# Optimization experiments

Hardware: AMD Instinct MI355X
Metric: run time of the kernel (lower is better)

Reference implementation:

```python
import jax, jax.numpy as jnp
import numpy as np

NUM_USERS, NUM_ITEMS, RANK = 610, 193609, 4
BATCH = 2097152


def setup_inputs() -> dict:
    key = jax.random.key(0)
    ks = jax.random.split(key, 10)
    users = jax.random.randint(ks[0], (BATCH,), 0, NUM_USERS + 1)
    items = jax.random.randint(ks[1], (BATCH,), 0, NUM_ITEMS + 1)
    # embedding tables (nn.Embedding default init ~ N(0,1))
    embed_U = jax.random.normal(ks[2], (NUM_USERS + 1, RANK), dtype=jnp.float32)
    embed_V = jax.random.normal(ks[3], (NUM_ITEMS + 1, RANK), dtype=jnp.float32)
    # Linear params, Kaiming-uniform-ish scale (1/sqrt(fan_in))
    def lin(k, fan_in, fan_out):
        k1, k2 = jax.random.split(k)
        bound = 1.0 / np.sqrt(fan_in)
        W = jax.random.uniform(k1, (fan_out, fan_in), jnp.float32, -bound, bound)
        b = jax.random.uniform(k2, (fan_out,), jnp.float32, -bound, bound)
        return W, b
    W1, b1 = lin(ks[4], 2 * RANK, 50)
    W2, b2 = lin(ks[5], 50, 20)
    W3, b3 = lin(ks[6], 20, 1)
    return {"users": users, "items": items,
            "embed_U": embed_U, "embed_V": embed_V,
            "W1": W1, "b1": b1, "W2": W2, "b2": b2, "W3": W3, "b3": b3}


def reference(users, items, embed_U, embed_V, W1, b1, W2, b2, W3, b3):
    # Vectorized version of the per-sample loop: gather + concat + 3-layer MLP
    eu = embed_U[users]                      # [B, rank]
    ev = embed_V[items]                      # [B, rank]
    x = jnp.concatenate([eu, ev], axis=-1)   # [B, 2*rank]
    x = jax.nn.relu(x @ W1.T + b1)           # [B, 50]
    x = jax.nn.relu(x @ W2.T + b2)           # [B, 20]
    x = x @ W3.T + b3                        # [B, 1]
    return x[:, 0]                           # [B]
```

## Files before the change

### kernel.cpp

```cpp
#include <hip/hip_runtime.h>
#include <hip/hip_fp16.h>


typedef __attribute__((ext_vector_type(16))) float    f32x16;
typedef __attribute__((ext_vector_type(8)))  _Float16 f16x8;
typedef __attribute__((ext_vector_type(2)))  _Float16 f16x2;
typedef __attribute__((ext_vector_type(2)))  __fp16   h16x2;

#define H1 50
#define H2 20

union W4 { unsigned u[4]; f16x8 v; };
union W8 { _Float16 h[8]; f16x8 v; };

static __device__ inline unsigned pk_u32(float a, float b) {
    h16x2 p = __builtin_amdgcn_cvt_pkrtz(a, b);
    unsigned u; __builtin_memcpy(&u, &p, 4); return u;
}
static __device__ inline unsigned pkmax0(unsigned a) {
    unsigned r;
    asm("v_pk_max_f16 %0, %1, %2" : "=v"(r) : "v"(a), "v"(0u));
    return r;
}
static __device__ inline float dot2(unsigned a, unsigned b, float c) {
    f16x2 av, bv;
    __builtin_memcpy(&av, &a, 4);
    __builtin_memcpy(&bv, &b, 4);
    return __builtin_amdgcn_fdot2(av, bv, c, false);
}

__global__ __launch_bounds__(256, 4) void neumf_mfma32(
    const int* __restrict__ users, const int* __restrict__ items,
    const float* __restrict__ eU, const float* __restrict__ eV,
    const float* __restrict__ W1, const float* __restrict__ b1,
    const float* __restrict__ W2, const float* __restrict__ b2,
    const float* __restrict__ W3, const float* __restrict__ b3,
    float* __restrict__ out, int n, int nTiles, int tilesPerWave, int nU)
{
    const int lane = threadIdx.x & 63;
    const int wid  = blockIdx.x * (blockDim.x >> 6) + (threadIdx.x >> 6);
    const int h    = lane >> 5;
    const int r31  = lane & 31;

    __shared__ uint2 ldsU[616];
    for (int r = threadIdx.x; r < nU; r += 256) {
        float4 t = reinterpret_cast<const float4*>(eU)[r];
        ldsU[r] = make_uint2(pk_u32(t.x, t.y), pk_u32(t.z, t.w));
    }
    __syncthreads();

    f16x8 a1[2];
#pragma unroll
    for (int mt = 0; mt < 2; ++mt) {
        int m = 32 * mt + r31;
        float w[8] = {0.f,0.f,0.f,0.f,0.f,0.f,0.f,0.f};
        if (m < H1) {
#pragma unroll
            for (int i = 0; i < 4; ++i) w[i] = W1[m * 8 + 4 * h + i];
            if (h == 0) w[4] = b1[m];
        }
        W8 f;
#pragma unroll
        for (int i = 0; i < 8; ++i) f.h[i] = (_Float16)w[i];
        a1[mt] = f.v;
    }

    f16x8 a2[4];
    {
        int m = r31;
#pragma unroll
        for (int kt = 0; kt < 4; ++kt) {
            float w[8] = {0.f,0.f,0.f,0.f,0.f,0.f,0.f,0.f};
            if (m < H2) {
#pragma unroll
                for (int e = 0; e < 8; ++e) {
                    int k = 16 * kt + 4 * h + (e & 3) + 8 * (e >> 2);
                    if (k < H1)       w[e] = W2[m * H1 + k];
                    else if (k == H1) w[e] = b2[m];
                }
            }
            W8 f;
#pragma unroll
            for (int e = 0; e < 8; ++e) f.h[e] = (_Float16)w[e];
            a2[kt] = f.v;
        }
    }

    f16x8 a3;
    {
        W8 f;
#pragma unroll
        for (int e = 0; e < 8; ++e) {
            int k = 4 * h + (e & 3) + 8 * (e >> 2);
            f.h[e] = (_Float16)W3[k];
        }
        a3 = f.v;
    }
    const unsigned w3p0 = h ? 0u : pk_u32(W3[16], W3[17]);
    const unsigned w3p1 = h ? 0u : pk_u32(W3[18], W3[19]);
    const float bias3 = b3[0];

    const int*     ip  = h ? items : users;
    const unsigned w2c = h ? 0u : 0x00003C00u;

    const int t0 = wid * tilesPerWave;
    const int t1 = min(t0 + tilesPerWave, nTiles);
    if (t0 >= t1) return;
    const int tl = t1 - 1;

    int idx_cur = ip[32 * t0 + r31];
    float4 gv_cur;
    if (h) gv_cur = *reinterpret_cast<const float4*>(eV + 4 * (size_t)idx_cur);
    int idx_next = ip[32 * min(t0 + 1, tl) + r31];

#pragma unroll 2
    for (int T = t0; T < t1; ++T) {
        float4 gv_next;
        if (h) gv_next = *reinterpret_cast<const float4*>(eV + 4 * (size_t)idx_next);
        int idx_nn = ip[32 * min(T + 2, tl) + r31];

        uint2 cw;
        if (h) cw = make_uint2(pk_u32(gv_cur.x, gv_cur.y), pk_u32(gv_cur.z, gv_cur.w));
        else   cw = ldsU[idx_cur];

        W4 bf1;
        bf1.u[0] = cw.x;
        bf1.u[1] = cw.y;
        bf1.u[2] = w2c;
        bf1.u[3] = 0u;

        f32x16 z = {0.f,0.f,0.f,0.f,0.f,0.f,0.f,0.f,0.f,0.f,0.f,0.f,0.f,0.f,0.f,0.f};
        f32x16 d1[2];
        d1[0] = __builtin_amdgcn_mfma_f32_32x32x16_f16(a1[0], bf1.v, z, 0, 0, 0);
        d1[1] = __builtin_amdgcn_mfma_f32_32x32x16_f16(a1[1], bf1.v, z, 0, 0, 0);

        f32x16 d2 = z;
#pragma unroll
        for (int kt = 0; kt < 3; ++kt) {
            const int mt = kt >> 1, q = kt & 1;
            W4 bf;
#pragma unroll
            for (int j = 0; j < 4; ++j)
                bf.u[j] = pkmax0(pk_u32(d1[mt][8 * q + 2 * j], d1[mt][8 * q + 2 * j + 1]));
            d2 = __builtin_amdgcn_mfma_f32_32x32x16_f16(a2[kt], bf.v, d2, 0, 0, 0);
        }
        {
            W4 bf;
            bf.u[0] = pkmax0(pk_u32(d1[1][8], d1[1][9]));
            bf.u[1] = w2c;
            bf.u[2] = w2c;
            bf.u[3] = w2c;
            d2 = __builtin_amdgcn_mfma_f32_32x32x16_f16(a2[3], bf.v, d2, 0, 0, 0);
        }

        W4 b3f;
        b3f.u[0] = pkmax0(pk_u32(d2[0], d2[1]));
        b3f.u[1] = pkmax0(pk_u32(d2[2], d2[3]));
        b3f.u[2] = pkmax0(pk_u32(d2[4], d2[5]));
        b3f.u[3] = pkmax0(pk_u32(d2[6], d2[7]));
        f32x16 d3 = __builtin_amdgcn_mfma_f32_32x32x16_f16(a3, b3f.v, z, 0, 0, 0);

        unsigned t0w = pkmax0(pk_u32(d2[8],  d2[9]));
        unsigned t1w = pkmax0(pk_u32(d2[10], d2[11]));
        float pt = dot2(t0w, w3p0, dot2(t1w, w3p1, bias3));

        if (!h) out[32 * T + r31] = d3[0] + pt;

        gv_cur = gv_next; idx_cur = idx_next; idx_next = idx_nn;
    }
}

extern "C" void kernel_launch(void* const* d_in, const int* in_sizes, int n_in,
                              void* d_out, int out_size, void* d_ws, size_t ws_size,
                              hipStream_t stream) {
    const int*   users = (const int*)d_in[0];
    const int*   items = (const int*)d_in[1];
    const float* eU    = (const float*)d_in[2];
    const float* eV    = (const float*)d_in[3];
    const float* W1    = (const float*)d_in[4];
    const float* b1    = (const float*)d_in[5];
    const float* W2    = (const float*)d_in[6];
    const float* b2    = (const float*)d_in[7];
    const float* W3    = (const float*)d_in[8];
    const float* b3    = (const float*)d_in[9];
    float*       out   = (float*)d_out;

    int n  = in_sizes[0];
    int nU = in_sizes[2] / 4;

    int nTiles = (n + 31) / 32;
    int blocks = 1024, threads = 256;
    int totalWaves = blocks * (threads / 64);
    int tilesPerWave = (nTiles + totalWaves - 1) / totalWaves;
    neumf_mfma32<<<blocks, threads, 0, stream>>>(users, items, eU, eV,
                                                 W1, b1, W2, b2, W3, b3,
                                                 out, n, nTiles, tilesPerWave, nU);
}
```

Before: 23.60 us.

## Process two 32-sample tiles per iteration to interleave independent MFMA chains

Each wave iteration now handles two independent 32-row tiles (A and B) and interleaves their MFMA chains, so one tile's MFMAs can issue while the other's dependent results are pending. Outputs are merged with a cross-half shuffle so all 64 lanes write a contiguous 64-element store instead of half the lanes writing 32. Launch bounds drop to 3 waves/SIMD and the grid goes from 1024 to 768 blocks to fit the higher register use. The cost is more VGPR pressure and lower occupancy, which may reduce latency hiding for the embedding gathers.

```diff
diff --git a/kernel.cpp b/kernel.cpp
--- a/kernel.cpp
+++ b/kernel.cpp
@@ -29,13 +29,13 @@
     return __builtin_amdgcn_fdot2(av, bv, c, false);
 }
 
-__global__ __launch_bounds__(256, 4) void neumf_mfma32(
+__global__ __launch_bounds__(256, 3) void neumf_dual(
     const int* __restrict__ users, const int* __restrict__ items,
     const float* __restrict__ eU, const float* __restrict__ eV,
     const float* __restrict__ W1, const float* __restrict__ b1,
     const float* __restrict__ W2, const float* __restrict__ b2,
     const float* __restrict__ W3, const float* __restrict__ b3,
-    float* __restrict__ out, int n, int nTiles, int tilesPerWave, int nU)
+    float* __restrict__ out, int n, int nIter, int itersPerWave, int nU)
 {
     const int lane = threadIdx.x & 63;
     const int wid  = blockIdx.x * (blockDim.x >> 6) + (threadIdx.x >> 6);
@@ -103,70 +103,102 @@
     const int*     ip  = h ? items : users;
     const unsigned w2c = h ? 0u : 0x00003C00u;
 
-    const int t0 = wid * tilesPerWave;
-    const int t1 = min(t0 + tilesPerWave, nTiles);
+    const int t0 = wid * itersPerWave;
+    const int t1 = min(t0 + itersPerWave, nIter);
     if (t0 >= t1) return;
     const int tl = t1 - 1;
 
-    int idx_cur = ip[32 * t0 + r31];
-    float4 gv_cur;
-    if (h) gv_cur = *reinterpret_cast<const float4*>(eV + 4 * (size_t)idx_cur);
-    int idx_next = ip[32 * min(t0 + 1, tl) + r31];
-
-#pragma unroll 2
+    int iA_cur = ip[64 * t0 + r31];
+    int iB_cur = ip[64 * t0 + 32 + r31];
+    float4 gvA_cur, gvB_cur;
+    if (h) {
+        gvA_cur = *reinterpret_cast<const float4*>(eV + 4 * (size_t)iA_cur);
+        gvB_cur = *reinterpret_cast<const float4*>(eV + 4 * (size_t)iB_cur);
+    }
+    int iA_next = ip[64 * min(t0 + 1, tl) + r31];
+    int iB_next = ip[64 * min(t0 + 1, tl) + 32 + r31];
+
     for (int T = t0; T < t1; ++T) {
-        float4 gv_next;
-        if (h) gv_next = *reinterpret_cast<const float4*>(eV + 4 * (size_t)idx_next);
-        int idx_nn = ip[32 * min(T + 2, tl) + r31];
-
-        uint2 cw;
-        if (h) cw = make_uint2(pk_u32(gv_cur.x, gv_cur.y), pk_u32(gv_cur.z, gv_cur.w));
-        else   cw = ldsU[idx_cur];
-
-        W4 bf1;
-        bf1.u[0] = cw.x;
-        bf1.u[1] = cw.y;
-        bf1.u[2] = w2c;
-        bf1.u[3] = 0u;
+        float4 gvA_next, gvB_next;
+        if (h) {
+            gvA_next = *reinterpret_cast<const float4*>(eV + 4 * (size_t)iA_next);
+            gvB_next = *reinterpret_cast<const float4*>(eV + 4 * (size_t)iB_next);
+        }
+        int iA_nn = ip[64 * min(T + 2, tl) + r31];
+        int iB_nn = ip[64 * min(T + 2, tl) + 32 + r31];
+
+        uint2 cwA, cwB;
+        if (h) {
+            cwA = make_uint2(pk_u32(gvA_cur.x, gvA_cur.y), pk_u32(gvA_cur.z, gvA_cur.w));
+            cwB = make_uint2(pk_u32(gvB_cur.x, gvB_cur.y), pk_u32(gvB_cur.z, gvB_cur.w));
+        } else {
+            cwA = ldsU[iA_cur];
+            cwB = ldsU[iB_cur];
+        }
+
+        W4 bfA, bfB;
+        bfA.u[0] = cwA.x; bfA.u[1] = cwA.y; bfA.u[2] = w2c; bfA.u[3] = 0u;
+        bfB.u[0] = cwB.x; bfB.u[1] = cwB.y; bfB.u[2] = w2c; bfB.u[3] = 0u;
 
         f32x16 z = {0.f,0.f,0.f,0.f,0.f,0.f,0.f,0.f,0.f,0.f,0.f,0.f,0.f,0.f,0.f,0.f};
-        f32x16 d1[2];
-        d1[0] = __builtin_amdgcn_mfma_f32_32x32x16_f16(a1[0], bf1.v, z, 0, 0, 0);
-        d1[1] = __builtin_amdgcn_mfma_f32_32x32x16_f16(a1[1], bf1.v, z, 0, 0, 0);
-
-        f32x16 d2 = z;
+        f32x16 d1A0 = __builtin_amdgcn_mfma_f32_32x32x16_f16(a1[0], bfA.v, z, 0, 0, 0);
+        f32x16 d1B0 = __builtin_amdgcn_mfma_f32_32x32x16_f16(a1[0], bfB.v, z, 0, 0, 0);
+        f32x16 d1A1 = __builtin_amdgcn_mfma_f32_32x32x16_f16(a1[1], bfA.v, z, 0, 0, 0);
+        f32x16 d1B1 = __builtin_amdgcn_mfma_f32_32x32x16_f16(a1[1], bfB.v, z, 0, 0, 0);
+
+        f32x16 d2A = z, d2B = z;
 #pragma unroll
         for (int kt = 0; kt < 3; ++kt) {
-            const int mt = kt >> 1, q = kt & 1;
-            W4 bf;
-#pragma unroll
-            for (int j = 0; j < 4; ++j)
-                bf.u[j] = pkmax0(pk_u32(d1[mt][8 * q + 2 * j], d1[mt][8 * q + 2 * j + 1]));
-            d2 = __builtin_amdgcn_mfma_f32_32x32x16_f16(a2[kt], bf.v, d2, 0, 0, 0);
+            const int q = kt & 1;
+            const f32x16& sA = (kt < 2) ? d1A0 : d1A1;
+            const f32x16& sB = (kt < 2) ? d1B0 : d1B1;
+            W4 bA, bB;
+#pragma unroll
+            for (int j = 0; j < 4; ++j) {
+                bA.u[j] = pkmax0(pk_u32(sA[8*q + 2*j], sA[8*q + 2*j + 1]));
+                bB.u[j] = pkmax0(pk_u32(sB[8*q + 2*j], sB[8*q + 2*j + 1]));
+            }
+            d2A = __builtin_amdgcn_mfma_f32_32x32x16_f16(a2[kt], bA.v, d2A, 0, 0, 0);
+            d2B = __builtin_amdgcn_mfma_f32_32x32x16_f16(a2[kt], bB.v, d2B, 0, 0, 0);
         }
         {
-            W4 bf;
-            bf.u[0] = pkmax0(pk_u32(d1[1][8], d1[1][9]));
-            bf.u[1] = w2c;
-            bf.u[2] = w2c;
-            bf.u[3] = w2c;
-            d2 = __builtin_amdgcn_mfma_f32_32x32x16_f16(a2[3], bf.v, d2, 0, 0, 0);
-        }
-
-        W4 b3f;
-        b3f.u[0] = pkmax0(pk_u32(d2[0], d2[1]));
-        b3f.u[1] = pkmax0(pk_u32(d2[2], d2[3]));
-        b3f.u[2] = pkmax0(pk_u32(d2[4], d2[5]));
-        b3f.u[3] = pkmax0(pk_u32(d2[6], d2[7]));
-        f32x16 d3 = __builtin_amdgcn_mfma_f32_32x32x16_f16(a3, b3f.v, z, 0, 0, 0);
-
-        unsigned t0w = pkmax0(pk_u32(d2[8],  d2[9]));
-        unsigned t1w = pkmax0(pk_u32(d2[10], d2[11]));
-        float pt = dot2(t0w, w3p0, dot2(t1w, w3p1, bias3));
-
-        if (!h) out[32 * T + r31] = d3[0] + pt;
-
-        gv_cur = gv_next; idx_cur = idx_next; idx_next = idx_nn;
+            W4 bA, bB;
+            bA.u[0] = pkmax0(pk_u32(d1A1[8], d1A1[9]));
+            bB.u[0] = pkmax0(pk_u32(d1B1[8], d1B1[9]));
+            bA.u[1] = w2c; bA.u[2] = w2c; bA.u[3] = w2c;
+            bB.u[1] = w2c; bB.u[2] = w2c; bB.u[3] = w2c;
+            d2A = __builtin_amdgcn_mfma_f32_32x32x16_f16(a2[3], bA.v, d2A, 0, 0, 0);
+            d2B = __builtin_amdgcn_mfma_f32_32x32x16_f16(a2[3], bB.v, d2B, 0, 0, 0);
+        }
+
+        W4 b3fA, b3fB;
+        b3fA.u[0] = pkmax0(pk_u32(d2A[0], d2A[1]));
+        b3fA.u[1] = pkmax0(pk_u32(d2A[2], d2A[3]));
+        b3fA.u[2] = pkmax0(pk_u32(d2A[4], d2A[5]));
+        b3fA.u[3] = pkmax0(pk_u32(d2A[6], d2A[7]));
+        b3fB.u[0] = pkmax0(pk_u32(d2B[0], d2B[1]));
+        b3fB.u[1] = pkmax0(pk_u32(d2B[2], d2B[3]));
+        b3fB.u[2] = pkmax0(pk_u32(d2B[4], d2B[5]));
+        b3fB.u[3] = pkmax0(pk_u32(d2B[6], d2B[7]));
+        f32x16 d3A = __builtin_amdgcn_mfma_f32_32x32x16_f16(a3, b3fA.v, z, 0, 0, 0);
+        f32x16 d3B = __builtin_amdgcn_mfma_f32_32x32x16_f16(a3, b3fB.v, z, 0, 0, 0);
+
+        unsigned tA0 = pkmax0(pk_u32(d2A[8],  d2A[9]));
+        unsigned tA1 = pkmax0(pk_u32(d2A[10], d2A[11]));
+        unsigned tB0 = pkmax0(pk_u32(d2B[8],  d2B[9]));
+        unsigned tB1 = pkmax0(pk_u32(d2B[10], d2B[11]));
+        float ptA = dot2(tA0, w3p0, dot2(tA1, w3p1, bias3));
+        float ptB = dot2(tB0, w3p0, dot2(tB1, w3p1, bias3));
+
+        float outA = d3A[0] + ptA;
+        float outB = d3B[0] + ptB;
+        float outBs = __shfl_xor(outB, 32, 64);
+
+        out[64 * T + lane] = h ? outBs : outA;
+
+        gvA_cur = gvA_next; gvB_cur = gvB_next;
+        iA_cur = iA_next;   iB_cur = iB_next;
+        iA_next = iA_nn;    iB_next = iB_nn;
     }
 }
 
@@ -188,11 +220,11 @@
     int n  = in_sizes[0];
     int nU = in_sizes[2] / 4;
 
-    int nTiles = (n + 31) / 32;
-    int blocks = 1024, threads = 256;
+    int nIter = (n + 63) / 64;
+    int blocks = 768, threads = 256;
     int totalWaves = blocks * (threads / 64);
-    int tilesPerWave = (nTiles + totalWaves - 1) / totalWaves;
-    neumf_mfma32<<<blocks, threads, 0, stream>>>(users, items, eU, eV,
-                                                 W1, b1, W2, b2, W3, b3,
-                                                 out, n, nTiles, tilesPerWave, nU);
-}
+    int itersPerWave = (nIter + totalWaves - 1) / totalWaves;
+    neumf_dual<<<blocks, threads, 0, stream>>>(users, items, eU, eV,
+                                               W1, b1, W2, b2, W3, b3,
+                                               out, n, nIter, itersPerWave, nU);
+}
```

Measured after the change: 25.38 us. +7.5%, slower.
